# Kernel tuning notes

Measured on AMD Instinct MI355X. Metric: run time of the kernel, lower is better.

## Reference

```python
import jax, jax.numpy as jnp
import numpy as np

N_NODES = 100000
N_EDGES = 1600000
NUM_GRAPHS = 128
ATOM_IN = 92
FEA = 64          # atom_fea_len
EDGE_DIM = 41
Z_DIM = 2 * FEA + EDGE_DIM  # 169, CGConv concat [x_i, x_j, edge_attr]
N_CONV = 5
HID = 256
LATENT = 128
CH = 3
BN_EPS = 1e-5


def setup_inputs() -> dict:
    key = jax.random.key(0)
    ks = jax.random.split(key, 16)
    x = jax.random.normal(ks[0], (N_NODES, ATOM_IN), dtype=jnp.float32)
    edge_index = jax.random.randint(ks[1], (2, N_EDGES), 0, N_NODES, dtype=jnp.int64)
    edge_attr = jax.random.uniform(ks[2], (N_EDGES, EDGE_DIM), dtype=jnp.float32)
    batch = jnp.sort(jax.random.randint(ks[3], (N_NODES,), 0, NUM_GRAPHS, dtype=jnp.int64))

    def lin(k, fan_in, fan_out):
        kw, kb = jax.random.split(k)
        bound = 1.0 / np.sqrt(fan_in)
        W = jax.random.uniform(kw, (fan_in, fan_out), jnp.float32, -bound, bound)
        b = jax.random.uniform(kb, (fan_out,), jnp.float32, -bound, bound)
        return W, b

    emb_W, emb_b = lin(ks[4], ATOM_IN, FEA)
    # stacked per-layer CGConv params: [N_CONV, ...]
    fW, fb, sW, sb = [], [], [], []
    for i in range(N_CONV):
        Wf, bf = lin(jax.random.fold_in(ks[5], i), Z_DIM, FEA)
        Ws, bs = lin(jax.random.fold_in(ks[6], i), Z_DIM, FEA)
        fW.append(Wf); fb.append(bf); sW.append(Ws); sb.append(bs)
    lin_f_W = jnp.stack(fW); lin_f_b = jnp.stack(fb)
    lin_s_W = jnp.stack(sW); lin_s_b = jnp.stack(sb)
    bn_gamma = jnp.ones((N_CONV, FEA), jnp.float32)
    bn_beta = jnp.zeros((N_CONV, FEA), jnp.float32)

    head_W1, head_b1 = lin(ks[7], FEA, HID)
    head_W2, head_b2 = lin(ks[8], HID, HID)
    head_W3, head_b3 = lin(ks[9], HID, LATENT * CH)
    return dict(x=x, edge_index=edge_index, edge_attr=edge_attr, batch=batch,
                emb_W=emb_W, emb_b=emb_b,
                lin_f_W=lin_f_W, lin_f_b=lin_f_b, lin_s_W=lin_s_W, lin_s_b=lin_s_b,
                bn_gamma=bn_gamma, bn_beta=bn_beta,
                head_W1=head_W1, head_b1=head_b1, head_W2=head_W2, head_b2=head_b2,
                head_W3=head_W3, head_b3=head_b3)


def _cgconv(h, src, dst, edge_attr, Wf, bf, Ws, bs, gamma, beta):
    # PyG CGConv: z = cat([x_i, x_j, edge_attr]); msg = sigmoid(lin_f(z)) * softplus(lin_s(z))
    # aggr='add' at target i (= edge_index[1]); batch_norm (training stats); residual.
    z = jnp.concatenate([h[dst], h[src], edge_attr], axis=-1)  # [E, 169]
    msg = jax.nn.sigmoid(z @ Wf + bf) * jax.nn.softplus(z @ Ws + bs)  # [E, 64]
    agg = jax.ops.segment_sum(msg, dst, num_segments=h.shape[0])  # [N, 64]
    mu = agg.mean(axis=0)
    var = agg.var(axis=0)  # biased, as in torch BN normalization
    out = (agg - mu) * jax.lax.rsqrt(var + BN_EPS) * gamma + beta
    return out + h


def reference(x, edge_index, edge_attr, batch,
              emb_W, emb_b, lin_f_W, lin_f_b, lin_s_W, lin_s_b, bn_gamma, bn_beta,
              head_W1, head_b1, head_W2, head_b2, head_W3, head_b3):
    src, dst = edge_index[0], edge_index[1]  # x_j = source, x_i = target
    h = x @ emb_W + emb_b  # [N, 64]
    for i in range(N_CONV):
        h = _cgconv(h, src, dst, edge_attr,
                    lin_f_W[i], lin_f_b[i], lin_s_W[i], lin_s_b[i],
                    bn_gamma[i], bn_beta[i])
    # global_mean_pool over graphs
    sums = jax.ops.segment_sum(h, batch, num_segments=NUM_GRAPHS)
    cnts = jax.ops.segment_sum(jnp.ones((h.shape[0],), h.dtype), batch, num_segments=NUM_GRAPHS)
    pooled = sums / jnp.maximum(cnts, 1.0)[:, None]  # [G, 64]
    g = jax.nn.softplus(pooled @ head_W1 + head_b1)
    g = jax.nn.softplus(g @ head_W2 + head_b2)
    dos = g @ head_W3 + head_b3  # [G, 384]
    return dos.reshape(-1, CH, LATENT)
```

## Files before the change

kernel.cpp:

```cpp
#include <hip/hip_runtime.h>
#include <math.h>

#define N_NODES 100000
#define N_EDGES 1600000
#define NUM_GRAPHS 128
#define ATOM_IN 92
#define FEA 64
#define EDGE_DIM 41
#define ZDIM 169
#define KPAD 192
#define N_CONV 5
#define HID 256
#define OUT_PER_G 384
#define NPAD 100096
#define NBLK 391
#define ESTRIDE 200

#define HBYTES ((size_t)N_NODES * FEA * 4)

typedef __attribute__((ext_vector_type(8))) short bf16x8;
typedef __attribute__((ext_vector_type(4))) float f32x4;

__device__ __forceinline__ float sigmoidf_(float x) {
    return 1.0f / (1.0f + __expf(-x));
}
__device__ __forceinline__ float softplusf_(float x) {
    float a = fabsf(x);
    return fmaxf(x, 0.0f) + __logf(1.0f + __expf(-a));
}
__device__ __forceinline__ unsigned short f2bf(float f) {
    unsigned int u = __float_as_uint(f);
    u = (u + 0x7FFFu + ((u >> 16) & 1u)) >> 16;
    return (unsigned short)u;
}

__global__ __launch_bounds__(256) void k_embed(const float* __restrict__ x,
                                               const float* __restrict__ W,
                                               const float* __restrict__ b,
                                               float* __restrict__ h,
                                               unsigned short* __restrict__ hb) {
    int idx = blockIdx.x * 256 + threadIdx.x;
    int c = idx & 63;
    int n = __builtin_amdgcn_readfirstlane(idx >> 6);
    float acc = 0.0f;
#pragma unroll 4
    for (int k = 0; k < ATOM_IN; ++k)
        acc = fmaf(x[n * ATOM_IN + k], W[k * FEA + c], acc);
    acc += b[c];
    h[idx] = acc;
    hb[idx] = f2bf(acc);
}

__global__ __launch_bounds__(256) void k_hist(const int* __restrict__ dst,
                                              int* __restrict__ cnt) {
    int e = blockIdx.x * 256 + threadIdx.x;
    if (e < N_EDGES) atomicAdd(&cnt[dst[e]], 1);
}

__global__ __launch_bounds__(256) void k_blocksum(const int* __restrict__ cnt,
                                                  int* __restrict__ bsum) {
    __shared__ int s[256];
    int t = threadIdx.x;
    s[t] = cnt[blockIdx.x * 256 + t];
    __syncthreads();
    for (int o = 128; o > 0; o >>= 1) {
        if (t < o) s[t] += s[t + o];
        __syncthreads();
    }
    if (t == 0) bsum[blockIdx.x] = s[0];
}

__global__ __launch_bounds__(512) void k_topscan(int* __restrict__ bsum) {
    __shared__ int s[512];
    int t = threadIdx.x;
    int v = (t < NBLK) ? bsum[t] : 0;
    s[t] = v;
    __syncthreads();
    for (int o = 1; o < 512; o <<= 1) {
        int x = (t >= o) ? s[t - o] : 0;
        __syncthreads();
        s[t] += x;
        __syncthreads();
    }
    if (t < NBLK) bsum[t] = s[t] - v;
}

__global__ __launch_bounds__(256) void k_localscan(const int* __restrict__ cnt,
                                                   const int* __restrict__ bsum,
                                                   int* __restrict__ offs) {
    __shared__ int s[256];
    int t = threadIdx.x;
    int i = blockIdx.x * 256 + t;
    int v = cnt[i];
    s[t] = v;
    __syncthreads();
    for (int o = 1; o < 256; o <<= 1) {
        int x = (t >= o) ? s[t - o] : 0;
        __syncthreads();
        s[t] += x;
        __syncthreads();
    }
    offs[i] = bsum[blockIdx.x] + s[t] - v;
}

__global__ __launch_bounds__(256) void k_scatter_ea(const int* __restrict__ dst,
                                                    const int* __restrict__ src,
                                                    const float* __restrict__ ea,
                                                    const int* __restrict__ offs,
                                                    int* __restrict__ cursor,
                                                    int* __restrict__ dstS,
                                                    int* __restrict__ srcS,
                                                    unsigned short* __restrict__ eaSb) {
    __shared__ int p_sh[256];
    int t = threadIdx.x;
    int e = blockIdx.x * 256 + t;
    int d = dst[e];
    int p = offs[d] + atomicAdd(&cursor[d], 1);
    dstS[p] = d;
    srcS[p] = src[e];
    p_sh[t] = p;
    __syncthreads();

    int row = t >> 3, j = t & 7;
#pragma unroll
    for (int i = 0; i < 8; ++i, row += 32) {
        int ge = blockIdx.x * 256 + row;
        int pp = p_sh[row];
        const float* srcp = ea + (size_t)ge * EDGE_DIM;
        unsigned short outv[8];
#pragma unroll
        for (int q = 0; q < 8; ++q) {
            int col = j * 8 + q;
            float v = (col < EDGE_DIM) ? srcp[col] : 0.0f;
            outv[q] = f2bf(v);
        }
        *(uint4*)&eaSb[(size_t)pp * 64 + j * 8] = *(uint4*)outv;
    }
}

__global__ __launch_bounds__(256) void k_wprep(const float* __restrict__ lfW,
                                               const float* __restrict__ lsW,
                                               unsigned short* __restrict__ WbT) {
    int idx = blockIdx.x * 256 + threadIdx.x;
    if (idx >= N_CONV * 128 * KPAD) return;
    int k = idx % KPAD;
    int c = (idx / KPAD) % 128;
    int L = idx / (KPAD * 128);
    float v = 0.0f;
    if (k < ZDIM) {
        const float* W = ((c < 64) ? lfW : lsW) + (size_t)L * ZDIM * FEA;
        v = W[k * FEA + (c & 63)];
    }
    WbT[idx] = f2bf(v);
}

__global__ __launch_bounds__(256) void k_edge(const unsigned short* __restrict__ hb,
                                              const int* __restrict__ dstS,
                                              const int* __restrict__ srcS,
                                              const unsigned short* __restrict__ eaSb,
                                              const unsigned short* __restrict__ WbT,
                                              const float* __restrict__ bfv,
                                              const float* __restrict__ bsv,
                                              float* __restrict__ agg) {
    __shared__ unsigned short z[64 * ESTRIDE];
    __shared__ int dsh[64], ssh[64];
    __shared__ float biasf[64], biass[64];
    float* msg = (float*)z;

    int t = threadIdx.x;
    int l = t & 63;
    int w = t >> 6;
    int eb = blockIdx.x * 64;

    if (t < 64) {
        dsh[t] = dstS[eb + t];
        ssh[t] = srcS[eb + t];
        biasf[t] = bfv[t];
    } else if (t < 128) {
        biass[t - 64] = bsv[t - 64];
    }
    __syncthreads();

    {
        int sub = l >> 3, j = l & 7;
#pragma unroll
        for (int i = 0; i < 6; ++i) {
            int idx = i * 32 + w * 8 + sub;
            int e = idx & 63, sec = idx >> 6;
            const unsigned short* srcp =
                (sec == 0) ? hb + (size_t)dsh[e] * 64
              : (sec == 1) ? hb + (size_t)ssh[e] * 64
                           : eaSb + (size_t)(eb + e) * 64;
            *(uint4*)&z[e * ESTRIDE + sec * 64 + j * 8] =
                *(const uint4*)&srcp[j * 8];
        }
    }
    __syncthreads();

    int lm = l & 15, lg = l >> 4;
    int col = w * 16 + lm;
    f32x4 accF[4] = {};
    f32x4 accS[4] = {};
#pragma unroll 1
    for (int ks = 0; ks < 6; ++ks) {
        int kofs = ks * 32 + lg * 8;
        bf16x8 a[4];
#pragma unroll
        for (int r = 0; r < 4; ++r)
            a[r] = *(const bf16x8*)&z[(16 * r + lm) * ESTRIDE + kofs];
        bf16x8 bF = *(const bf16x8*)&WbT[(size_t)col * KPAD + kofs];
        bf16x8 bS = *(const bf16x8*)&WbT[(size_t)(64 + col) * KPAD + kofs];
#pragma unroll
        for (int r = 0; r < 4; ++r) {
            accF[r] = __builtin_amdgcn_mfma_f32_16x16x32_bf16(a[r], bF, accF[r], 0, 0, 0);
            accS[r] = __builtin_amdgcn_mfma_f32_16x16x32_bf16(a[r], bS, accS[r], 0, 0, 0);
        }
    }
    __syncthreads();

    {
        float bfc = biasf[col], bsc = biass[col];
#pragma unroll
        for (int r = 0; r < 4; ++r)
#pragma unroll
            for (int j = 0; j < 4; ++j) {
                int e = 16 * r + 4 * lg + j;
                msg[e * 66 + col] =
                    sigmoidf_(accF[r][j] + bfc) * softplusf_(accS[r][j] + bsc);
            }
    }
    __syncthreads();

    {
        int e0 = w * 16;
        int cur = __builtin_amdgcn_readfirstlane(dsh[e0]);
        float a = 0.0f;
        for (int e = e0; e < e0 + 16; ++e) {
            a += msg[e * 66 + l];
            int nxt = (e + 1 < e0 + 16) ? __builtin_amdgcn_readfirstlane(dsh[e + 1]) : -1;
            if (nxt != cur) {
                atomicAdd(&agg[(size_t)cur * FEA + l], a);
                a = 0.0f;
                cur = nxt;
            }
        }
    }
}

__global__ __launch_bounds__(256) void k_bnstats(const float* __restrict__ agg,
                                                 float* __restrict__ stats) {
    int t = threadIdx.x, c = t & 63, w = t >> 6;
    float s = 0.0f, q = 0.0f;
    for (int r = blockIdx.x * 4 + w; r < N_NODES; r += gridDim.x * 4) {
        float v = agg[(size_t)r * FEA + c];
        s += v;
        q = fmaf(v, v, q);
    }
    __shared__ float red[2][256];
    red[0][t] = s;
    red[1][t] = q;
    __syncthreads();
    if (t < 64) {
        s = red[0][t] + red[0][t + 64] + red[0][t + 128] + red[0][t + 192];
        q = red[1][t] + red[1][t + 64] + red[1][t + 128] + red[1][t + 192];
        atomicAdd(&stats[t], s);
        atomicAdd(&stats[64 + t], q);
    }
}

__global__ __launch_bounds__(256) void k_bnapply(const float* __restrict__ agg,
                                                 const float* __restrict__ stats,
                                                 const float* __restrict__ gamma,
                                                 const float* __restrict__ beta,
                                                 float* __restrict__ h,
                                                 unsigned short* __restrict__ hb) {
    int idx = blockIdx.x * 256 + threadIdx.x;
    int c = idx & 63;
    float mu = stats[c] * (1.0f / N_NODES);
    float var = stats[64 + c] * (1.0f / N_NODES) - mu * mu;
    float rs = rsqrtf(var + 1e-5f);
    float v = agg[idx];
    float hn = h[idx] + (v - mu) * rs * gamma[c] + beta[c];
    h[idx] = hn;
    hb[idx] = f2bf(hn);
}

__global__ __launch_bounds__(256) void k_pool(const float* __restrict__ h,
                                              const int* __restrict__ batch,
                                              float* __restrict__ psum,
                                              float* __restrict__ pcnt) {
    int g = blockIdx.x;
    int lo, hi;
    {
        int a = 0, b = N_NODES;
        while (a < b) { int m = (a + b) >> 1; if (batch[m] < g) a = m + 1; else b = m; }
        lo = a;
    }
    {
        int a = lo, b = N_NODES;
        while (a < b) { int m = (a + b) >> 1; if (batch[m] < g + 1) a = m + 1; else b = m; }
        hi = a;
    }
    int t = threadIdx.x, c = t & 63, w = t >> 6;
    float s = 0.0f;
    for (int r = lo + w; r < hi; r += 4) s += h[(size_t)r * FEA + c];
    __shared__ float red[256];
    red[t] = s;
    __syncthreads();
    if (t < 64) {
        psum[g * FEA + t] = red[t] + red[t + 64] + red[t + 128] + red[t + 192];
        if (t == 0) pcnt[g] = (float)(hi - lo);
    }
}

__global__ __launch_bounds__(256) void k_head(const float* __restrict__ psum,
                                              const float* __restrict__ pcnt,
                                              const float* __restrict__ W1, const float* __restrict__ b1,
                                              const float* __restrict__ W2, const float* __restrict__ b2,
                                              const float* __restrict__ W3, const float* __restrict__ b3,
                                              float* __restrict__ out) {
    int g = blockIdx.x, t = threadIdx.x;
    __shared__ float p[64], g1[256], g2[256];
    if (t < 64) p[t] = psum[g * FEA + t] / fmaxf(pcnt[g], 1.0f);
    __syncthreads();
    {
        float acc = b1[t];
#pragma unroll 8
        for (int k = 0; k < FEA; ++k) acc = fmaf(p[k], W1[k * HID + t], acc);
        g1[t] = softplusf_(acc);
    }
    __syncthreads();
    {
        float acc = b2[t];
#pragma unroll 8
        for (int k = 0; k < HID; ++k) acc = fmaf(g1[k], W2[k * HID + t], acc);
        g2[t] = softplusf_(acc);
    }
    __syncthreads();
    for (int c = t; c < OUT_PER_G; c += 256) {
        float acc = b3[c];
#pragma unroll 8
        for (int k = 0; k < HID; ++k) acc = fmaf(g2[k], W3[k * OUT_PER_G + c], acc);
        out[g * OUT_PER_G + c] = acc;
    }
}

extern "C" void kernel_launch(void* const* d_in, const int* in_sizes, int n_in,
                              void* d_out, int out_size, void* d_ws, size_t ws_size,
                              hipStream_t stream) {
    (void)in_sizes; (void)n_in; (void)out_size; (void)ws_size;
    const float* x    = (const float*)d_in[0];
    const int*   ei   = (const int*)d_in[1];
    const float* ea   = (const float*)d_in[2];
    const int*   batch= (const int*)d_in[3];
    const float* embW = (const float*)d_in[4];
    const float* embB = (const float*)d_in[5];
    const float* lfW  = (const float*)d_in[6];
    const float* lfB  = (const float*)d_in[7];
    const float* lsW  = (const float*)d_in[8];
    const float* lsB  = (const float*)d_in[9];
    const float* gam  = (const float*)d_in[10];
    const float* bet  = (const float*)d_in[11];
    const float* W1 = (const float*)d_in[12];
    const float* b1 = (const float*)d_in[13];
    const float* W2 = (const float*)d_in[14];
    const float* b2 = (const float*)d_in[15];
    const float* W3 = (const float*)d_in[16];
    const float* b3 = (const float*)d_in[17];

    const int* srcI = ei;
    const int* dstI = ei + N_EDGES;

    char* ws = (char*)d_ws;
    size_t off = 0;
    float* h      = (float*)(ws + off); off += HBYTES;
    float* agg    = (float*)(ws + off); off += HBYTES;
    float* stats  = (float*)(ws + off); off += 512;
    float* psum   = (float*)(ws + off); off += 32768;
    float* pcnt   = (float*)(ws + off); off += 512;
    unsigned short* hbuf = (unsigned short*)(ws + off); off += (size_t)N_NODES * 64 * 2;
    unsigned short* eaSb = (unsigned short*)(ws + off); off += (size_t)N_EDGES * 64 * 2;
    unsigned short* WbT  = (unsigned short*)(ws + off); off += (size_t)N_CONV * 128 * KPAD * 2;
    int*   cnt    = (int*)(ws + off);   off += (size_t)NPAD * 4;
    int*   bsum   = (int*)(ws + off);   off += 2048;
    int*   offs   = (int*)(ws + off);   off += (size_t)NPAD * 4;
    int*   cursor = (int*)(ws + off);   off += (size_t)NPAD * 4;
    int*   dstS   = (int*)(ws + off);   off += (size_t)N_EDGES * 4;
    int*   srcS   = (int*)(ws + off);   off += (size_t)N_EDGES * 4;

    hipMemsetAsync(cnt, 0, (size_t)NPAD * 4, stream);
    hipMemsetAsync(cursor, 0, (size_t)NPAD * 4, stream);
    k_hist<<<(N_EDGES + 255) / 256, 256, 0, stream>>>(dstI, cnt);
    k_blocksum<<<NBLK, 256, 0, stream>>>(cnt, bsum);
    k_topscan<<<1, 512, 0, stream>>>(bsum);
    k_localscan<<<NBLK, 256, 0, stream>>>(cnt, bsum, offs);
    k_scatter_ea<<<N_EDGES / 256, 256, 0, stream>>>(dstI, srcI, ea, offs, cursor,
                                                    dstS, srcS, eaSb);
    k_wprep<<<(N_CONV * 128 * KPAD + 255) / 256, 256, 0, stream>>>(lfW, lsW, WbT);

    k_embed<<<N_NODES * FEA / 256, 256, 0, stream>>>(x, embW, embB, h, hbuf);

    for (int L = 0; L < N_CONV; ++L) {
        hipMemsetAsync(agg, 0, HBYTES + 512, stream);
        k_edge<<<N_EDGES / 64, 256, 0, stream>>>(hbuf, dstS, srcS, eaSb,
                                                 WbT + (size_t)L * 128 * KPAD,
                                                 lfB + L * FEA, lsB + L * FEA,
                                                 agg);
        k_bnstats<<<256, 256, 0, stream>>>(agg, stats);
        k_bnapply<<<N_NODES * FEA / 256, 256, 0, stream>>>(agg, stats,
                                                           gam + L * FEA, bet + L * FEA,
                                                           h, hbuf);
    }

    k_pool<<<NUM_GRAPHS, 256, 0, stream>>>(h, batch, psum, pcnt);
    k_head<<<NUM_GRAPHS, 256, 0, stream>>>(psum, pcnt, W1, b1, W2, b2, W3, b3,
                                           (float*)d_out);
}
```

Measured before the change: 1.701 ms.

## Read edge attrs directly into MFMA regs, shrink LDS tile, fold agg zeroing into bnapply

The edge kernel stages only the gathered destination and source node rows in LDS, which shrinks the row stride and the shared footprint. The two edge-attribute K-steps load their A fragments straight from global memory into registers. Bias loads move to registers, one barrier is dropped, and the K loop is fully unrolled. The per-layer memset of agg is replaced by zeroing inside k_bnapply plus a small stats memset, which saves a full memset pass per layer; the risk is uncoalesced 16-byte global A-fragment reads.

```diff
diff --git a/kernel.cpp b/kernel.cpp
--- a/kernel.cpp
+++ b/kernel.cpp
@@ -14,7 +14,7 @@
 #define OUT_PER_G 384
 #define NPAD 100096
 #define NBLK 391
-#define ESTRIDE 200
+#define ESTRIDE 136
 
 #define HBYTES ((size_t)N_NODES * FEA * 4)
 
@@ -163,8 +163,7 @@
                                               const float* __restrict__ bsv,
                                               float* __restrict__ agg) {
     __shared__ unsigned short z[64 * ESTRIDE];
-    __shared__ int dsh[64], ssh[64];
-    __shared__ float biasf[64], biass[64];
+    __shared__ int dsh[64];
     float* msg = (float*)z;
 
     int t = threadIdx.x;
@@ -172,54 +171,65 @@
     int w = t >> 6;
     int eb = blockIdx.x * 64;
 
-    if (t < 64) {
-        dsh[t] = dstS[eb + t];
-        ssh[t] = srcS[eb + t];
-        biasf[t] = bfv[t];
-    } else if (t < 128) {
-        biass[t - 64] = bsv[t - 64];
-    }
-    __syncthreads();
-
-    {
-        int sub = l >> 3, j = l & 7;
-#pragma unroll
-        for (int i = 0; i < 6; ++i) {
-            int idx = i * 32 + w * 8 + sub;
-            int e = idx & 63, sec = idx >> 6;
-            const unsigned short* srcp =
-                (sec == 0) ? hb + (size_t)dsh[e] * 64
-              : (sec == 1) ? hb + (size_t)ssh[e] * 64
-                           : eaSb + (size_t)(eb + e) * 64;
-            *(uint4*)&z[e * ESTRIDE + sec * 64 + j * 8] =
-                *(const uint4*)&srcp[j * 8];
-        }
+    if (t < 64) dsh[t] = dstS[eb + t];
+
+    {
+        int e0 = (w << 3) + (l >> 3);
+        int j = l & 7;
+        int n0 = dstS[eb + e0], n1 = dstS[eb + e0 + 32];
+        int s0 = srcS[eb + e0], s1 = srcS[eb + e0 + 32];
+        *(uint4*)&z[e0 * ESTRIDE + j * 8] =
+            *(const uint4*)&hb[(size_t)n0 * 64 + j * 8];
+        *(uint4*)&z[(e0 + 32) * ESTRIDE + j * 8] =
+            *(const uint4*)&hb[(size_t)n1 * 64 + j * 8];
+        *(uint4*)&z[e0 * ESTRIDE + 64 + j * 8] =
+            *(const uint4*)&hb[(size_t)s0 * 64 + j * 8];
+        *(uint4*)&z[(e0 + 32) * ESTRIDE + 64 + j * 8] =
+            *(const uint4*)&hb[(size_t)s1 * 64 + j * 8];
     }
     __syncthreads();
 
     int lm = l & 15, lg = l >> 4;
     int col = w * 16 + lm;
+    const unsigned short* WF = WbT + (size_t)col * KPAD;
+    const unsigned short* WS = WbT + (size_t)(64 + col) * KPAD;
     f32x4 accF[4] = {};
     f32x4 accS[4] = {};
-#pragma unroll 1
-    for (int ks = 0; ks < 6; ++ks) {
+#pragma unroll
+    for (int ks = 0; ks < 4; ++ks) {
         int kofs = ks * 32 + lg * 8;
         bf16x8 a[4];
 #pragma unroll
         for (int r = 0; r < 4; ++r)
             a[r] = *(const bf16x8*)&z[(16 * r + lm) * ESTRIDE + kofs];
-        bf16x8 bF = *(const bf16x8*)&WbT[(size_t)col * KPAD + kofs];
-        bf16x8 bS = *(const bf16x8*)&WbT[(size_t)(64 + col) * KPAD + kofs];
+        bf16x8 bF = *(const bf16x8*)&WF[kofs];
+        bf16x8 bS = *(const bf16x8*)&WS[kofs];
 #pragma unroll
         for (int r = 0; r < 4; ++r) {
             accF[r] = __builtin_amdgcn_mfma_f32_16x16x32_bf16(a[r], bF, accF[r], 0, 0, 0);
             accS[r] = __builtin_amdgcn_mfma_f32_16x16x32_bf16(a[r], bS, accS[r], 0, 0, 0);
         }
     }
-    __syncthreads();
-
-    {
-        float bfc = biasf[col], bsc = biass[col];
+#pragma unroll
+    for (int ks = 0; ks < 2; ++ks) {
+        int kofs = 128 + ks * 32 + lg * 8;
+        bf16x8 a[4];
+#pragma unroll
+        for (int r = 0; r < 4; ++r)
+            a[r] = *(const bf16x8*)&eaSb[(size_t)(eb + 16 * r + lm) * 64 +
+                                         ks * 32 + lg * 8];
+        bf16x8 bF = *(const bf16x8*)&WF[kofs];
+        bf16x8 bS = *(const bf16x8*)&WS[kofs];
+#pragma unroll
+        for (int r = 0; r < 4; ++r) {
+            accF[r] = __builtin_amdgcn_mfma_f32_16x16x32_bf16(a[r], bF, accF[r], 0, 0, 0);
+            accS[r] = __builtin_amdgcn_mfma_f32_16x16x32_bf16(a[r], bS, accS[r], 0, 0, 0);
+        }
+    }
+    __syncthreads();
+
+    {
+        float bfc = bfv[col], bsc = bsv[col];
 #pragma unroll
         for (int r = 0; r < 4; ++r)
 #pragma unroll
@@ -268,7 +278,7 @@
     }
 }
 
-__global__ __launch_bounds__(256) void k_bnapply(const float* __restrict__ agg,
+__global__ __launch_bounds__(256) void k_bnapply(float* __restrict__ agg,
                                                  const float* __restrict__ stats,
                                                  const float* __restrict__ gamma,
                                                  const float* __restrict__ beta,
@@ -280,6 +290,7 @@
     float var = stats[64 + c] * (1.0f / N_NODES) - mu * mu;
     float rs = rsqrtf(var + 1e-5f);
     float v = agg[idx];
+    agg[idx] = 0.0f;
     float hn = h[idx] + (v - mu) * rs * gamma[c] + beta[c];
     h[idx] = hn;
     hb[idx] = f2bf(hn);
@@ -400,8 +411,10 @@
 
     k_embed<<<N_NODES * FEA / 256, 256, 0, stream>>>(x, embW, embB, h, hbuf);
 
+    hipMemsetAsync(agg, 0, HBYTES + 512, stream);
+
     for (int L = 0; L < N_CONV; ++L) {
-        hipMemsetAsync(agg, 0, HBYTES + 512, stream);
+        if (L > 0) hipMemsetAsync(stats, 0, 512, stream);
         k_edge<<<N_EDGES / 64, 256, 0, stream>>>(hbuf, dstS, srcS, eaSb,
                                                  WbT + (size_t)L * 128 * KPAD,
                                                  lfB + L * FEA, lsB + L * FEA,
```

New measurement: 1.954 ms. 14.9% more time.
